# Performance work log

Hardware: AMD Instinct MI355X
Metric: run time of the kernel (lower is better)

## Reference

```python
import jax, jax.numpy as jnp
import numpy as np

SDIM, VDIM, HID, DEPTH = 128, 3, 64, 4
N, E = 50000, 800000
CUTOFF = 5.0


def setup_inputs() -> dict:
    key = jax.random.key(0)
    ks = jax.random.split(key, 16)
    s = jax.random.normal(ks[0], (N, SDIM), jnp.float32)
    v = jax.random.normal(ks[1], (N, 3, VDIM), jnp.float32)
    edge_index = jax.random.randint(ks[2], (2, E), 0, N, dtype=jnp.int32).astype(jnp.int64)
    d = jax.random.uniform(ks[3], (E,), jnp.float32) * CUTOFF
    r = jax.random.normal(ks[4], (E, 3), jnp.float32)
    r = r / jnp.linalg.norm(r, axis=-1, keepdims=True)
    batch = jnp.zeros((N,), jnp.int64)

    def w(k, shape):
        return jax.random.normal(k, shape, jnp.float32) / jnp.sqrt(jnp.float32(shape[-2]))

    return {
        's': s, 'v': v, 'edge_index': edge_index, 'd': d, 'r': r, 'batch': batch,
        'We1': w(ks[5], (DEPTH, 2 * SDIM + 1, HID)), 'be1': jnp.zeros((DEPTH, HID), jnp.float32),
        'We2': w(ks[6], (DEPTH, HID, HID)), 'be2': jnp.zeros((DEPTH, HID), jnp.float32),
        'Wn1': w(ks[7], (DEPTH, SDIM + HID, HID)), 'bn1': jnp.zeros((DEPTH, HID), jnp.float32),
        'Wn2': w(ks[8], (DEPTH, HID, SDIM)), 'bn2': jnp.zeros((DEPTH, SDIM), jnp.float32),
        'Wv': w(ks[9], (DEPTH, HID, 2 * VDIM)), 'bv': jnp.zeros((DEPTH, 2 * VDIM), jnp.float32),
    }


def _egcl(s, v, src, dst, d, r, C, deg, We1, be1, We2, be2, Wn1, bn1, Wn2, bn2, Wv, bv):
    n = s.shape[0]
    # edge message MLP on gathered endpoint features + distance
    x = jnp.concatenate([s[dst], s[src], d[:, None]], axis=-1)   # [E, 2*SDIM+1]
    h = jax.nn.silu(x @ We1 + be1)
    h = jax.nn.silu(h @ We2 + be2)
    h = h * C[:, None]                                            # cutoff envelope
    # scalar update
    agg_s = jax.ops.segment_sum(h, dst, num_segments=n)           # [N, HID]
    u = jax.nn.silu(jnp.concatenate([s, agg_s], axis=-1) @ Wn1 + bn1)
    s = s + (u @ Wn2 + bn2)
    # equivariant vector update: gated neighbor vectors + gated edge directions
    gates = h @ Wv + bv                                           # [E, 2*VDIM]
    g1, g2 = gates[:, :VDIM], gates[:, VDIM:]
    mv = v[src] * g1[:, None, :] + r[:, :, None] * g2[:, None, :] # [E, 3, VDIM]
    agg_v = jax.ops.segment_sum(mv, dst, num_segments=n) / deg[:, None, None]  # mean aggr
    v = v + agg_v
    return s, v


def reference(s, v, edge_index, d, r, batch, We1, be1, We2, be2, Wn1, bn1, Wn2, bn2, Wv, bv):
    src, dst = edge_index[0], edge_index[1]
    C = 0.5 * (jnp.cos(jnp.pi * d / CUTOFF) + 1.0) * (d < CUTOFF).astype(d.dtype)
    deg = jax.ops.segment_sum(jnp.ones_like(d), dst, num_segments=s.shape[0])
    deg = jnp.maximum(deg, 1.0)
    for i in range(DEPTH):
        s, v = _egcl(s, v, src, dst, d, r, C, deg,
                     We1[i], be1[i], We2[i], be2[i],
                     Wn1[i], bn1[i], Wn2[i], bn2[i], Wv[i], bv[i])
    return (s, v)
```

## Files before the change

### kernel.cpp

```cpp
#include <hip/hip_runtime.h>
#include <math.h>

#define SDIM 128
#define HID 64
#define DEPTH 4
#define CUTOFF_F 5.0f
#define CHUNK 4096

typedef __attribute__((ext_vector_type(8))) short bf16x8;
typedef __attribute__((ext_vector_type(4))) float f32x4;
typedef float4 __attribute__((aligned(4))) float4_u;

__device__ __forceinline__ float silu_f(float x) {
    float e = __expf(-x);
    return x * __builtin_amdgcn_rcpf(1.0f + e);
}

__device__ __forceinline__ unsigned short f2bf(float x) {
    __bf16 b = (__bf16)x;
    return __builtin_bit_cast(unsigned short, b);
}
__device__ __forceinline__ unsigned int f2bf2(float a, float b) {
    return (unsigned int)f2bf(a) | ((unsigned int)f2bf(b) << 16);
}
// ... 92 lines not shown
    for (int base = base0; base < base0 + CHUNK; base += 256) {
        int i = base + t;
        int v = (i < N) ? deg_i[i] : 0;
        int incl = v;
#pragma unroll
        for (int off = 1; off < 64; off <<= 1) {
            int x = __shfl_up(incl, off, 64);
            if (lane >= off) incl += x;
        }
        if (lane == 63) wsum[w] = incl;
        __syncthreads();
        int wpre = 0;
#pragma unroll
        for (int k = 0; k < 4; ++k) if (k < w) wpre += wsum[k];
        int total = wsum[0] + wsum[1] + wsum[2] + wsum[3];
        int carry = carry_s;
        if (i < N) row_start[i] = carry + wpre + incl - v;
        __syncthreads();
        if (t == 0) carry_s = carry + total;
        __syncthreads();
    }
}

__global__ void scatter_kernel(const int* __restrict__ srcw, const int* __restrict__ dstw,
                               const float* __restrict__ dvec, const float* __restrict__ rvec,
                               const int* __restrict__ row_start, int* __restrict__ cursor,
                               float* __restrict__ rec, int E) {
    int e = blockIdx.x * blockDim.x + threadIdx.x;
    if (e >= E) return;
    int dd = dstw[e];
    int ofs = atomicAdd(&cursor[dd], 1);
    int pos = row_start[dd] + ofs;
    float dv = dvec[e];
    float c = 0.5f * (cosf(3.14159265358979323846f * dv * (1.0f / CUTOFF_F)) + 1.0f);
    c = (dv < CUTOFF_F) ? c : 0.0f;
    float4 r0 = make_float4(__int_as_float(srcw[e]), __int_as_float(dd), dv, c);
    float4 r1 = make_float4(rvec[(size_t)e * 3 + 0], rvec[(size_t)e * 3 + 1],
                            rvec[(size_t)e * 3 + 2], 0.0f);
    *(float4*)(rec + (size_t)pos * 8)     = r0;
    *(float4*)(rec + (size_t)pos * 8 + 4) = r1;
}

__global__ __launch_bounds__(256) void wprep_kernel(
    const float* __restrict__ We1, const float* __restrict__ We2,
    const float* __restrict__ Wv,  const float* __restrict__ Wn1,
    const float* __restrict__ Wn2,
    unsigned short* __restrict__ We1t, unsigned short* __restrict__ We2t,
    unsigned short* __restrict__ Wvt,  unsigned short* __restrict__ Wn1t,
    unsigned short* __restrict__ Wn2t) {
    int l = blockIdx.x, t = threadIdx.x;
    const float* W2 = We2 + (size_t)l * HID * HID;
    unsigned short* T2 = We2t + (size_t)l * HID * HID;
    for (int idx = t; idx < HID * HID; idx += 256) {
        int n = idx >> 6, k = idx & 63;
        T2[n * 64 + k] = f2bf(W2[k * HID + n]);
    }
    const float* Wvl = Wv + (size_t)l * HID * 6;
    unsigned short* Tv = Wvt + (size_t)l * 16 * 64;
    for (int idx = t; idx < 16 * 64; idx += 256) {
        int n = idx >> 6, k = idx & 63;
        Tv[idx] = (n < 6) ? f2bf(Wvl[k * 6 + n]) : (unsigned short)0;
    }
    const float* W1 = We1 + (size_t)l * 257 * 64;
    unsigned short* T1 = We1t + (size_t)l * 128 * 128;
    for (int idx = t; idx < 128 * 128; idx += 256) {
        int n = idx >> 7, k = idx & 127;
        float w = (n < 64) ? W1[(size_t)k * 64 + n] : W1[(size_t)(k + 128) * 64 + (n - 64)];
        T1[n * 128 + k] = f2bf(w);
    }
    const float* Wn1l = Wn1 + (size_t)l * 192 * 64;
    unsigned short* Tn1 = Wn1t + (size_t)l * 64 * 192;
    for (int idx = t; idx < 64 * 192; idx += 256) {
        int n = idx / 192, k = idx - n * 192;
        Tn1[idx] = f2bf(Wn1l[(size_t)k * 64 + n]);
    }
    const float* Wn2l = Wn2 + (size_t)l * 64 * 128;
    unsigned short* Tn2 = Wn2t + (size_t)l * 128 * 64;
    for (int idx = t; idx < 128 * 64; idx += 256) {
        int n = idx >> 6, k = idx & 63;
        Tn2[idx] = f2bf(Wn2l[(size_t)k * 128 + n]);
    }
}

__global__ __launch_bounds__(256) void node_pre_kernel(
    const float* __restrict__ s, const unsigned short* __restrict__ We1t,
    const float* __restrict__ be1,
    unsigned short* __restrict__ Pa, unsigned short* __restrict__ Pb, int N)
{
    __shared__ unsigned short sa[4][16 * 136];
    int t = threadIdx.x;
    int lane = t & 63, w = t >> 6;
    int n0 = blockIdx.x * 64;
    int m0 = w * 16;
    unsigned short* sw = sa[w];
    for (int idx = lane; idx < 512; idx += 64) {
        int rl = idx >> 5, c4 = (idx & 31) << 2;
        int n = n0 + m0 + rl;
        float4 val = make_float4(0.f, 0.f, 0.f, 0.f);
        if (n < N) val = *(const float4*)(s + (size_t)n * SDIM + c4);
        *(uint2*)(sw + rl * 136 + c4) = make_uint2(f2bf2(val.x, val.y), f2bf2(val.z, val.w));
    }
    __builtin_amdgcn_wave_barrier();
    int lm = lane & 15, lq = lane >> 4;

    bf16x8 af[4];
#pragma unroll
    for (int kc = 0; kc < 4; ++kc)
        af[kc] = *(const bf16x8*)(sw + lm * 136 + kc * 32 + lq * 8);

#pragma unroll
    for (int ct = 0; ct < 8; ++ct) {
        int col = ct * 16 + lm;
        f32x4 acc = {0.f, 0.f, 0.f, 0.f};
#pragma unroll
        for (int kc = 0; kc < 4; ++kc) {
            bf16x8 b = *(const bf16x8*)(We1t + (size_t)col * 128 + kc * 32 + lq * 8);
            acc = __builtin_amdgcn_mfma_f32_16x16x32_bf16(af[kc], b, acc, 0, 0, 0);
        }
        float bias = (ct < 4) ? be1[col] : 0.0f;
#pragma unroll
        for (int g = 0; g < 4; ++g) {
            int n = n0 + m0 + lq * 4 + g;
            if (n < N) {
                if (ct < 4) Pa[(size_t)n * HID + col]        = f2bf(acc[g] + bias);
                else        Pb[(size_t)n * HID + (col - 64)] = f2bf(acc[g]);
            }
        }
    }
}

__global__ __launch_bounds__(256) void edge_kernel(
    const float* __restrict__ rec,
    const unsigned short* __restrict__ Pa, const unsigned short* __restrict__ Pb,
    const float* __restrict__ wd,
    const unsigned short* __restrict__ We2t, const float* __restrict__ be2,
    const unsigned short* __restrict__ Wvt, const float* __restrict__ bv,
    const float* __restrict__ v,
    float* __restrict__ agg_s, float* __restrict__ agg_v, int E)
{
    __shared__ unsigned short hb[64 * 72];
    __shared__ float  gl[64 * 8];
    __shared__ float  vb[64 * 12];
    __shared__ int    m_dst[64];
    __shared__ float  m_C[64];
    __shared__ float4 m_r4[64];
    int t = threadIdx.x;
    int e0 = blockIdx.x * 64;
    int lane = t & 63, w = t >> 6;
    int lm = lane & 15, lq = lane >> 4;
    int m0 = w * 16, rm = m0 + lm;
    int ka = lq * 8, kb = 32 + lq * 8;

    int e  = e0 + rm;
    int ec = min(e, E - 1);
    float4 r0 = *(const float4*)(rec + (size_t)ec * 8);
    int srcr = __float_as_int(r0.x);
    int dstr = __float_as_int(r0.y);
    float dv = r0.z;
    float Cr = (e < E) ? r0.w : 0.0f;

    const unsigned short* pa = Pa + (size_t)dstr * HID;
    const unsigned short* pb = Pb + (size_t)srcr * HID;
    bf16x8 ba0 = *(const bf16x8*)(pa + ka);
    bf16x8 bb0 = *(const bf16x8*)(pb + ka);
    bf16x8 ba1 = *(const bf16x8*)(pa + kb);
    bf16x8 bb1 = *(const bf16x8*)(pb + kb);
    f8 xw = load8(wd + ka), yw = load8(wd + kb);

    if (lq == 0) {
        m_dst[rm] = dstr;
        m_C[rm]   = Cr;
        m_r4[rm]  = *(const float4*)(rec + (size_t)ec * 8 + 4);
    }
    {
        const float* vr = v + (size_t)srcr * 9;
        if (lq < 2) {
            float4_u a = *(const float4_u*)(vr + lq * 4);
            *(float4*)(vb + rm * 12 + lq * 4) = make_float4(a.x, a.y, a.z, a.w);
        } else if (lq == 2) {
            vb[rm * 12 + 8] = vr[8];
        }
    }
    bf16x8 wv0 = *(const bf16x8*)(Wvt + (size_t)lm * 64 + ka);
    bf16x8 wv1 = *(const bf16x8*)(Wvt + (size_t)lm * 64 + kb);

    bf16x8 afr0, afr1;
    {
        float fa[8], fb[8], h1[8];
        unpack8(ba0, fa); unpack8(bb0, fb);
#pragma unroll
        for (int j = 0; j < 8; ++j) h1[j] = silu_f(fa[j] + fb[j] + dv * xw.v[j]);
        afr0 = pack8(h1);
        unpack8(ba1, fa); unpack8(bb1, fb);
#pragma unroll
        for (int j = 0; j < 8; ++j) h1[j] = silu_f(fa[j] + fb[j] + dv * yw.v[j]);
        afr1 = pack8(h1);
    }

    __builtin_amdgcn_wave_barrier();
    float cc[4];
#pragma unroll
    for (int g = 0; g < 4; ++g) cc[g] = m_C[m0 + lq * 4 + g];
#pragma unroll
    for (int t4 = 0; t4 < 4; ++t4) {
        int col = t4 * 16 + lm;
        bf16x8 b0 = *(const bf16x8*)(We2t + (size_t)col * 64 + ka);
        bf16x8 b1 = *(const bf16x8*)(We2t + (size_t)col * 64 + kb);
        f32x4 a = {0.f, 0.f, 0.f, 0.f};
        a = __builtin_amdgcn_mfma_f32_16x16x32_bf16(afr0, b0, a, 0, 0, 0);
        a = __builtin_amdgcn_mfma_f32_16x16x32_bf16(afr1, b1, a, 0, 0, 0);
        float bias = be2[col];
#pragma unroll
        for (int g = 0; g < 4; ++g) {
            int er = m0 + lq * 4 + g;
            hb[er * 72 + col] = f2bf(silu_f(a[g] + bias) * cc[g]);
        }
    }
    __builtin_amdgcn_wave_barrier();

    {
        bf16x8 hb0 = *(const bf16x8*)(hb + rm * 72 + ka);
        bf16x8 hb1 = *(const bf16x8*)(hb + rm * 72 + kb);
        f32x4 ga = {0.f, 0.f, 0.f, 0.f};
        ga = __builtin_amdgcn_mfma_f32_16x16x32_bf16(wv0, hb0, ga, 0, 0, 0);
        ga = __builtin_amdgcn_mfma_f32_16x16x32_bf16(wv1, hb1, ga, 0, 0, 0);
        int er2 = m0 + lm;
        if (lq == 0) {
            float4_u bb = *(const float4_u*)bv;
            *(float4*)(gl + er2 * 8) =
                make_float4(ga[0] + bb.x, ga[1] + bb.y, ga[2] + bb.z, ga[3] + bb.w);
        } else if (lq == 1) {
            gl[er2 * 8 + 4] = ga[0] + bv[4];
            gl[er2 * 8 + 5] = ga[1] + bv[5];
        }
    }

    {
        int c = lane;
        float acc = 0.f;
        int cur = m_dst[m0];
#pragma unroll 4
        for (int r = m0; r < m0 + 16; ++r) {
            int dr = m_dst[r];
            if (dr != cur) {
                atomicAdd(&agg_s[(size_t)cur * HID + c], acc);
                acc = 0.f; cur = dr;
            }
            acc += bf2f(hb[r * 72 + c]);
        }
        atomicAdd(&agg_s[(size_t)cur * HID + c], acc);
    }
    __builtin_amdgcn_wave_barrier();

    if (lane < 36) {
        int seg = lane / 9;
        int c = lane - seg * 9;
        int i = c / 3, j = c - i * 3;
        int r0v = m0 + seg * 4;
        const float* mrf = (const float*)m_r4;
        float acc = 0.f;
        int cur = m_dst[r0v];
#pragma unroll
        for (int r = 0; r < 4; ++r) {
            int rr = r0v + r;
            int dr = m_dst[rr];
            if (dr != cur) {
                atomicAdd(&agg_v[(size_t)cur * 9 + c], acc);
                acc = 0.f; cur = dr;
            }
            if (e0 + rr < E) {
                acc += vb[rr * 12 + c] * gl[rr * 8 + j]
                     + mrf[rr * 4 + i] * gl[rr * 8 + 3 + j];
            }
        }
        atomicAdd(&agg_v[(size_t)cur * 9 + c], acc);
    }
}

__global__ __launch_bounds__(256) void node_fused_kernel(
    float* __restrict__ s, float* __restrict__ vout,
    float* __restrict__ agg_s, float* __restrict__ agg_v,
    const int* __restrict__ row_start,
    const unsigned short* __restrict__ Wn1t, const float* __restrict__ bn1,
    const unsigned short* __restrict__ Wn2t, const float* __restrict__ bn2,
    const unsigned short* __restrict__ We1tn, const float* __restrict__ be1n,
    unsigned short* __restrict__ Pa, unsigned short* __restrict__ Pb,
    int N, int do_pre)
{
    __shared__ unsigned short xa[4][16 * 200];
    __shared__ unsigned short ub[64 * 72];
    int t = threadIdx.x;
    int lane = t & 63, w = t >> 6;
    int n0 = blockIdx.x * 64;
    int m0 = w * 16;
    unsigned short* xw = xa[w];

    for (int idx = lane; idx < 512; idx += 64) {
        int rl = idx >> 5, c4 = (idx & 31) << 2;
        int n = n0 + m0 + rl;
        float4 val = make_float4(0.f, 0.f, 0.f, 0.f);
        if (n < N) val = *(const float4*)(s + (size_t)n * SDIM + c4);
        *(uint2*)(xw + rl * 200 + c4) = make_uint2(f2bf2(val.x, val.y), f2bf2(val.z, val.w));
    }
    for (int idx = lane; idx < 256; idx += 64) {
        int rl = idx >> 4, c4 = (idx & 15) << 2;
        int n = n0 + m0 + rl;
        float4 val = make_float4(0.f, 0.f, 0.f, 0.f);
        if (n < N) {
            float* ap = agg_s + (size_t)n * HID + c4;
            val = *(const float4*)ap;
            *(float4*)ap = make_float4(0.f, 0.f, 0.f, 0.f);
        }
        *(uint2*)(xw + rl * 200 + 128 + c4) = make_uint2(f2bf2(val.x, val.y), f2bf2(val.z, val.w));
    }
    __builtin_amdgcn_wave_barrier();

    int lm = lane & 15, lq = lane >> 4;

    bf16x8 af[6];
#pragma unroll
    for (int kc = 0; kc < 6; ++kc)
        af[kc] = *(const bf16x8*)(xw + lm * 200 + kc * 32 + lq * 8);

#pragma unroll
    for (int ct = 0; ct < 4; ++ct) {
        int col = ct * 16 + lm;
        f32x4 acc = {0.f, 0.f, 0.f, 0.f};
#pragma unroll
        for (int kc = 0; kc < 6; ++kc) {
            bf16x8 b = *(const bf16x8*)(Wn1t + (size_t)col * 192 + kc * 32 + lq * 8);
            acc = __builtin_amdgcn_mfma_f32_16x16x32_bf16(af[kc], b, acc, 0, 0, 0);
        }
        float bias = bn1[col];
#pragma unroll
        for (int g = 0; g < 4; ++g) {
            int er = m0 + lq * 4 + g;
            ub[er * 72 + col] = f2bf(silu_f(acc[g] + bias));
        }
    }
    __builtin_amdgcn_wave_barrier();

    unsigned short* sa = xw;
    bf16x8 uf[2];
#pragma unroll
    for (int kc = 0; kc < 2; ++kc)
        uf[kc] = *(const bf16x8*)(ub + (m0 + lm) * 72 + kc * 32 + lq * 8);

#pragma unroll
    for (int ct = 0; ct < 8; ++ct) {
        int col = ct * 16 + lm;
        f32x4 acc = {0.f, 0.f, 0.f, 0.f};
#pragma unroll
        for (int kc = 0; kc < 2; ++kc) {
            bf16x8 b = *(const bf16x8*)(Wn2t + (size_t)col * 64 + kc * 32 + lq * 8);
            acc = __builtin_amdgcn_mfma_f32_16x16x32_bf16(uf[kc], b, acc, 0, 0, 0);
        }
        float bias = bn2[col];
#pragma unroll
        for (int g = 0; g < 4; ++g) {
            int erl = lq * 4 + g;
            int n = n0 + m0 + erl;
            if (n < N) {
                float* sp = s + (size_t)n * SDIM + col;
                float sv = *sp + acc[g] + bias;
                *sp = sv;
                sa[erl * 136 + col] = f2bf(sv);
            } else {
                sa[erl * 136 + col] = 0;
            }
        }
    }
    __builtin_amdgcn_wave_barrier();

    if (do_pre) {
        bf16x8 pf[4];
#pragma unroll
        for (int kc = 0; kc < 4; ++kc)
            pf[kc] = *(const bf16x8*)(sa + lm * 136 + kc * 32 + lq * 8);

#pragma unroll
        for (int ct = 0; ct < 8; ++ct) {
            int col = ct * 16 + lm;
            f32x4 acc = {0.f, 0.f, 0.f, 0.f};
#pragma unroll
            for (int kc = 0; kc < 4; ++kc) {
                bf16x8 b = *(const bf16x8*)(We1tn + (size_t)col * 128 + kc * 32 + lq * 8);
                acc = __builtin_amdgcn_mfma_f32_16x16x32_bf16(pf[kc], b, acc, 0, 0, 0);
            }
            float bias = (ct < 4) ? be1n[col] : 0.0f;
#pragma unroll
            for (int g = 0; g < 4; ++g) {
                int n = n0 + m0 + lq * 4 + g;
                if (n < N) {
                    if (ct < 4) Pa[(size_t)n * HID + col]        = f2bf(acc[g] + bias);
                    else        Pb[(size_t)n * HID + (col - 64)] = f2bf(acc[g]);
                }
            }
        }
    }

    for (int idx = lane; idx < 144; idx += 64) {
        int rl = idx / 9, c = idx - rl * 9;
        int n2 = n0 + m0 + rl;
        if (n2 < N) {
            float av = agg_v[(size_t)n2 * 9 + c];
            agg_v[(size_t)n2 * 9 + c] = 0.f;
            float dg = fmaxf((float)(row_start[n2 + 1] - row_start[n2]), 1.0f);
            vout[(size_t)n2 * 9 + c] += av / dg;
        }
    }
}

extern "C" void kernel_launch(void* const* d_in, const int* in_sizes, int n_in,
                              void* d_out, int out_size, void* d_ws, size_t ws_size,
                              hipStream_t stream)
{
    const float* s_in  = (const float*)d_in[0];
    const float* v_in  = (const float*)d_in[1];
    const void*  ei    = d_in[2];
    const float* d_vec = (const float*)d_in[3];
    const float* r_vec = (const float*)d_in[4];
    const float* We1 = (const float*)d_in[6];
    const float* be1 = (const float*)d_in[7];
    const float* We2 = (const float*)d_in[8];
    const float* be2 = (const float*)d_in[9];
    const float* Wn1 = (const float*)d_in[10];
    const float* bn1 = (const float*)d_in[11];
    const float* Wn2 = (const float*)d_in[12];
    const float* bn2 = (const float*)d_in[13];
    const float* Wv  = (const float*)d_in[14];
    const float* bv  = (const float*)d_in[15];

    int N = in_sizes[0] / SDIM;
    int E = in_sizes[3];

    float* out_s = (float*)d_out;
    float* out_v = out_s + (size_t)N * SDIM;

    char* wp = (char*)d_ws;
    auto alloc = [&wp](size_t bytes) -> char* {
        char* p = wp;
        wp += (bytes + 31) & ~(size_t)31;
        return p;
    };
    float* rec       = (float*)alloc((size_t)E * 8 * 4);
    unsigned short* Pa = (unsigned short*)alloc((size_t)N * HID * 2);
    unsigned short* Pb = (unsigned short*)alloc((size_t)N * HID * 2);
    float* agg_s     = (float*)alloc((size_t)N * HID * 4);
    float* agg_v     = (float*)alloc((size_t)N * 9 * 4);
    int*   deg_i     = (int*)alloc((size_t)N * 4);
    int*   cursor    = (int*)alloc((size_t)N * 4);
    int*   row_start = (int*)alloc((size_t)(N + 1) * 4);
    int*   part      = (int*)alloc(64 * 4);
    int*   flag      = (int*)alloc(16);
    int*   srcw      = (int*)alloc((size_t)E * 4);
    int*   dstw      = (int*)alloc((size_t)E * 4);
    unsigned short* We2t = (unsigned short*)alloc((size_t)DEPTH * HID * HID * 2);
    unsigned short* Wvt  = (unsigned short*)alloc((size_t)DEPTH * 16 * 64 * 2);
    unsigned short* We1t = (unsigned short*)alloc((size_t)DEPTH * 128 * 128 * 2);
    unsigned short* Wn1t = (unsigned short*)alloc((size_t)DEPTH * 64 * 192 * 2);
    unsigned short* Wn2t = (unsigned short*)alloc((size_t)DEPTH * 128 * 64 * 2);

    hipMemcpyAsync(out_s, s_in, (size_t)N * SDIM * sizeof(float),
                   hipMemcpyDeviceToDevice, stream);
    hipMemcpyAsync(out_v, v_in, (size_t)N * 9 * sizeof(float),
                   hipMemcpyDeviceToDevice, stream);

    detect_idx_kernel<<<1, 64, 0, stream>>>(ei, N, flag);
    hipMemsetAsync(deg_i, 0, (size_t)N * 2 * sizeof(int), stream);
    hipMemsetAsync(agg_s, 0, (size_t)N * (HID + 9) * sizeof(float), stream);
    decode_idx_kernel<<<(2 * E + 255) / 256, 256, 0, stream>>>(ei, E, N, flag,
                                                               srcw, dstw, deg_i);
    int B1 = (N + CHUNK - 1) / CHUNK;
    scan1_kernel<<<B1, 256, 0, stream>>>(deg_i, part, N);
    scan2_kernel<<<1, 64, 0, stream>>>(part, row_start, B1, N);
    scan3_kernel<<<B1, 256, 0, stream>>>(deg_i, part, row_start, N);
    scatter_kernel<<<(E + 255) / 256, 256, 0, stream>>>(srcw, dstw, d_vec, r_vec,
                                                        row_start, cursor, rec, E);
    wprep_kernel<<<DEPTH, 256, 0, stream>>>(We1, We2, Wv, Wn1, Wn2,
                                            We1t, We2t, Wvt, Wn1t, Wn2t);

    int nb_n = (N + 63) / 64;
    int nb_e = (E + 63) / 64;
    node_pre_kernel<<<nb_n, 256, 0, stream>>>(out_s, We1t, be1, Pa, Pb, N);
    for (int l = 0; l < DEPTH; ++l) {
        int ln = (l + 1 < DEPTH) ? (l + 1) : 0;
        const float* We1_l = We1 + (size_t)l * 257 * 64;
        const float* be2_l = be2 + (size_t)l * 64;
        const float* bn1_l = bn1 + (size_t)l * 64;
        const float* bn2_l = bn2 + (size_t)l * 128;
        const float* bv_l  = bv  + (size_t)l * 6;
        const float* be1_n = be1 + (size_t)ln * 64;
        const unsigned short* We2t_l = We2t + (size_t)l * HID * HID;
        const unsigned short* Wvt_l  = Wvt  + (size_t)l * 16 * 64;
        const unsigned short* Wn1t_l = Wn1t + (size_t)l * 64 * 192;
        const unsigned short* Wn2t_l = Wn2t + (size_t)l * 128 * 64;
        const unsigned short* We1t_n = We1t + (size_t)ln * 128 * 128;

        edge_kernel<<<nb_e, 256, 0, stream>>>(rec, Pa, Pb,
                                              We1_l + 256 * 64,
                                              We2t_l, be2_l, Wvt_l, bv_l,
                                              out_v, agg_s, agg_v, E);
        node_fused_kernel<<<nb_n, 256, 0, stream>>>(out_s, out_v, agg_s, agg_v,
                                                    row_start,
                                                    Wn1t_l, bn1_l, Wn2t_l, bn2_l,
                                                    We1t_n, be1_n, Pa, Pb,
                                                    N, (l + 1 < DEPTH) ? 1 : 0);
    }
}
```

Baseline: 815.3 us.

## Make edge kernel persistent with double-buffered gather prefetch; shrink node blocks

```diff
diff --git a/kernel.cpp b/kernel.cpp
--- a/kernel.cpp
+++ b/kernel.cpp
@@ -198,23 +198,20 @@
     }
 }
 
-__global__ __launch_bounds__(256) void node_pre_kernel(
+__global__ __launch_bounds__(64) void node_pre_kernel(
     const float* __restrict__ s, const unsigned short* __restrict__ We1t,
     const float* __restrict__ be1,
     unsigned short* __restrict__ Pa, unsigned short* __restrict__ Pb, int N)
 {
-    __shared__ unsigned short sa[4][16 * 136];
-    int t = threadIdx.x;
-    int lane = t & 63, w = t >> 6;
-    int n0 = blockIdx.x * 64;
-    int m0 = w * 16;
-    unsigned short* sw = sa[w];
+    __shared__ unsigned short sa[16 * 136];
+    int lane = threadIdx.x;
+    int n0 = blockIdx.x * 16;
     for (int idx = lane; idx < 512; idx += 64) {
         int rl = idx >> 5, c4 = (idx & 31) << 2;
-        int n = n0 + m0 + rl;
+        int n = n0 + rl;
         float4 val = make_float4(0.f, 0.f, 0.f, 0.f);
         if (n < N) val = *(const float4*)(s + (size_t)n * SDIM + c4);
-        *(uint2*)(sw + rl * 136 + c4) = make_uint2(f2bf2(val.x, val.y), f2bf2(val.z, val.w));
+        *(uint2*)(sa + rl * 136 + c4) = make_uint2(f2bf2(val.x, val.y), f2bf2(val.z, val.w));
     }
     __builtin_amdgcn_wave_barrier();
     int lm = lane & 15, lq = lane >> 4;
@@ -222,7 +219,7 @@
     bf16x8 af[4];
 #pragma unroll
     for (int kc = 0; kc < 4; ++kc)
-        af[kc] = *(const bf16x8*)(sw + lm * 136 + kc * 32 + lq * 8);
+        af[kc] = *(const bf16x8*)(sa + lm * 136 + kc * 32 + lq * 8);
 
 #pragma unroll
     for (int ct = 0; ct < 8; ++ct) {
@@ -236,12 +233,44 @@
         float bias = (ct < 4) ? be1[col] : 0.0f;
 #pragma unroll
         for (int g = 0; g < 4; ++g) {
-            int n = n0 + m0 + lq * 4 + g;
+            int n = n0 + lq * 4 + g;
             if (n < N) {
                 if (ct < 4) Pa[(size_t)n * HID + col]        = f2bf(acc[g] + bias);
                 else        Pb[(size_t)n * HID + (col - 64)] = f2bf(acc[g]);
             }
         }
+    }
+}
+
+__device__ __forceinline__ void issue_tile(
+    float4 r0v, bool e_ok, const float* r4p,
+    int rm, int lq, int ka, int kb,
+    const unsigned short* __restrict__ Pa, const unsigned short* __restrict__ Pb,
+    const float* __restrict__ v,
+    bf16x8& ba0, bf16x8& bb0, bf16x8& ba1, bf16x8& bb1, float& dv_out,
+    int* m_dst, float* m_C, float4* m_r4, float* vb)
+{
+    int srcr = __float_as_int(r0v.x);
+    int dstr = __float_as_int(r0v.y);
+    dv_out = r0v.z;
+    float Cr = e_ok ? r0v.w : 0.0f;
+    const unsigned short* pa = Pa + (size_t)dstr * HID;
+    const unsigned short* pb = Pb + (size_t)srcr * HID;
+    ba0 = *(const bf16x8*)(pa + ka);
+    bb0 = *(const bf16x8*)(pb + ka);
+    ba1 = *(const bf16x8*)(pa + kb);
+    bb1 = *(const bf16x8*)(pb + kb);
+    if (lq == 0) {
+        m_dst[rm] = dstr;
+        m_C[rm]   = Cr;
+        m_r4[rm]  = *(const float4*)r4p;
+    }
+    const float* vr = v + (size_t)srcr * 9;
+    if (lq < 2) {
+        float4_u a = *(const float4_u*)(vr + lq * 4);
+        *(float4*)(vb + rm * 12 + lq * 4) = make_float4(a.x, a.y, a.z, a.w);
+    } else if (lq == 2) {
+        vb[rm * 12 + 8] = vr[8];
     }
 }
 
@@ -252,148 +281,155 @@
     const unsigned short* __restrict__ We2t, const float* __restrict__ be2,
     const unsigned short* __restrict__ Wvt, const float* __restrict__ bv,
     const float* __restrict__ v,
-    float* __restrict__ agg_s, float* __restrict__ agg_v, int E)
+    float* __restrict__ agg_s, float* __restrict__ agg_v,
+    int E, int ntiles, int tpb)
 {
     __shared__ unsigned short hb[64 * 72];
     __shared__ float  gl[64 * 8];
-    __shared__ float  vb[64 * 12];
-    __shared__ int    m_dst[64];
-    __shared__ float  m_C[64];
-    __shared__ float4 m_r4[64];
+    __shared__ float  vb2[2][64 * 12];
+    __shared__ int    m_dst2[2][64];
+    __shared__ float  m_C2[2][64];
+    __shared__ float4 m_r42[2][64];
+
     int t = threadIdx.x;
-    int e0 = blockIdx.x * 64;
     int lane = t & 63, w = t >> 6;
     int lm = lane & 15, lq = lane >> 4;
     int m0 = w * 16, rm = m0 + lm;
     int ka = lq * 8, kb = 32 + lq * 8;
 
-    int e  = e0 + rm;
-    int ec = min(e, E - 1);
-    float4 r0 = *(const float4*)(rec + (size_t)ec * 8);
-    int srcr = __float_as_int(r0.x);
-    int dstr = __float_as_int(r0.y);
-    float dv = r0.z;
-    float Cr = (e < E) ? r0.w : 0.0f;
-
-    const unsigned short* pa = Pa + (size_t)dstr * HID;
-    const unsigned short* pb = Pb + (size_t)srcr * HID;
-    bf16x8 ba0 = *(const bf16x8*)(pa + ka);
-    bf16x8 bb0 = *(const bf16x8*)(pb + ka);
-    bf16x8 ba1 = *(const bf16x8*)(pa + kb);
-    bf16x8 bb1 = *(const bf16x8*)(pb + kb);
+    int t0 = blockIdx.x * tpb;
+    int t1 = min(t0 + tpb, ntiles);
+    if (t0 >= t1) return;
+
     f8 xw = load8(wd + ka), yw = load8(wd + kb);
-
-    if (lq == 0) {
-        m_dst[rm] = dstr;
-        m_C[rm]   = Cr;
-        m_r4[rm]  = *(const float4*)(rec + (size_t)ec * 8 + 4);
-    }
-    {
-        const float* vr = v + (size_t)srcr * 9;
-        if (lq < 2) {
-            float4_u a = *(const float4_u*)(vr + lq * 4);
-            *(float4*)(vb + rm * 12 + lq * 4) = make_float4(a.x, a.y, a.z, a.w);
-        } else if (lq == 2) {
-            vb[rm * 12 + 8] = vr[8];
-        }
-    }
     bf16x8 wv0 = *(const bf16x8*)(Wvt + (size_t)lm * 64 + ka);
     bf16x8 wv1 = *(const bf16x8*)(Wvt + (size_t)lm * 64 + kb);
-
-    bf16x8 afr0, afr1;
+    float4_u bvv = *(const float4_u*)bv;
+    float bv4 = bv[4], bv5 = bv[5];
+
+    bf16x8 ba0, bb0, ba1, bb1;
+    float dv;
     {
-        float fa[8], fb[8], h1[8];
-        unpack8(ba0, fa); unpack8(bb0, fb);
-#pragma unroll
-        for (int j = 0; j < 8; ++j) h1[j] = silu_f(fa[j] + fb[j] + dv * xw.v[j]);
-        afr0 = pack8(h1);
-        unpack8(ba1, fa); unpack8(bb1, fb);
-#pragma unroll
-        for (int j = 0; j < 8; ++j) h1[j] = silu_f(fa[j] + fb[j] + dv * yw.v[j]);
-        afr1 = pack8(h1);
-    }
-
-    __builtin_amdgcn_wave_barrier();
-    float cc[4];
-#pragma unroll
-    for (int g = 0; g < 4; ++g) cc[g] = m_C[m0 + lq * 4 + g];
-#pragma unroll
-    for (int t4 = 0; t4 < 4; ++t4) {
-        int col = t4 * 16 + lm;
-        bf16x8 b0 = *(const bf16x8*)(We2t + (size_t)col * 64 + ka);
-        bf16x8 b1 = *(const bf16x8*)(We2t + (size_t)col * 64 + kb);
-        f32x4 a = {0.f, 0.f, 0.f, 0.f};
-        a = __builtin_amdgcn_mfma_f32_16x16x32_bf16(afr0, b0, a, 0, 0, 0);
-        a = __builtin_amdgcn_mfma_f32_16x16x32_bf16(afr1, b1, a, 0, 0, 0);
-        float bias = be2[col];
-#pragma unroll
-        for (int g = 0; g < 4; ++g) {
-            int er = m0 + lq * 4 + g;
-            hb[er * 72 + col] = f2bf(silu_f(a[g] + bias) * cc[g]);
-        }
-    }
-    __builtin_amdgcn_wave_barrier();
-
-    {
-        bf16x8 hb0 = *(const bf16x8*)(hb + rm * 72 + ka);
-        bf16x8 hb1 = *(const bf16x8*)(hb + rm * 72 + kb);
-        f32x4 ga = {0.f, 0.f, 0.f, 0.f};
-        ga = __builtin_amdgcn_mfma_f32_16x16x32_bf16(wv0, hb0, ga, 0, 0, 0);
-        ga = __builtin_amdgcn_mfma_f32_16x16x32_bf16(wv1, hb1, ga, 0, 0, 0);
-        int er2 = m0 + lm;
-        if (lq == 0) {
-            float4_u bb = *(const float4_u*)bv;
-            *(float4*)(gl + er2 * 8) =
-                make_float4(ga[0] + bb.x, ga[1] + bb.y, ga[2] + bb.z, ga[3] + bb.w);
-        } else if (lq == 1) {
-            gl[er2 * 8 + 4] = ga[0] + bv[4];
-            gl[er2 * 8 + 5] = ga[1] + bv[5];
-        }
-    }
-
-    {
-        int c = lane;
-        float acc = 0.f;
-        int cur = m_dst[m0];
+        int e  = t0 * 64 + rm;
+        int ec = min(e, E - 1);
+        float4 r0 = *(const float4*)(rec + (size_t)ec * 8);
+        int par0 = t0 & 1;
+        issue_tile(r0, e < E, rec + (size_t)ec * 8 + 4, rm, lq, ka, kb, Pa, Pb, v,
+                   ba0, bb0, ba1, bb1, dv,
+                   m_dst2[par0], m_C2[par0], m_r42[par0], vb2[par0]);
+    }
+
+    for (int itl = t0; itl < t1; ++itl) {
+        int par = itl & 1, npar = par ^ 1;
+        bool hasnext = (itl + 1 < t1);
+        int en  = (itl + 1) * 64 + rm;
+        int ecn = min(en, E - 1);
+        float4 r0n;
+        if (hasnext) r0n = *(const float4*)(rec + (size_t)ecn * 8);
+
+        bf16x8 afr0, afr1;
+        {
+            float fa[8], fb[8], h1[8];
+            unpack8(ba0, fa); unpack8(bb0, fb);
+#pragma unroll
+            for (int j = 0; j < 8; ++j) h1[j] = silu_f(fa[j] + fb[j] + dv * xw.v[j]);
+            afr0 = pack8(h1);
+            unpack8(ba1, fa); unpack8(bb1, fb);
+#pragma unroll
+            for (int j = 0; j < 8; ++j) h1[j] = silu_f(fa[j] + fb[j] + dv * yw.v[j]);
+            afr1 = pack8(h1);
+        }
+
+        float cc[4];
+#pragma unroll
+        for (int g = 0; g < 4; ++g) cc[g] = m_C2[par][m0 + lq * 4 + g];
+#pragma unroll
+        for (int t4 = 0; t4 < 4; ++t4) {
+            int col = t4 * 16 + lm;
+            bf16x8 b0 = *(const bf16x8*)(We2t + (size_t)col * 64 + ka);
+            bf16x8 b1 = *(const bf16x8*)(We2t + (size_t)col * 64 + kb);
+            f32x4 a = {0.f, 0.f, 0.f, 0.f};
+            a = __builtin_amdgcn_mfma_f32_16x16x32_bf16(afr0, b0, a, 0, 0, 0);
+            a = __builtin_amdgcn_mfma_f32_16x16x32_bf16(afr1, b1, a, 0, 0, 0);
+            float bias = be2[col];
+#pragma unroll
+            for (int g = 0; g < 4; ++g) {
+                int er = m0 + lq * 4 + g;
+                hb[er * 72 + col] = f2bf(silu_f(a[g] + bias) * cc[g]);
+            }
+        }
+        __builtin_amdgcn_wave_barrier();
+
+        {
+            bf16x8 hb0 = *(const bf16x8*)(hb + rm * 72 + ka);
+            bf16x8 hb1 = *(const bf16x8*)(hb + rm * 72 + kb);
+            f32x4 ga = {0.f, 0.f, 0.f, 0.f};
+            ga = __builtin_amdgcn_mfma_f32_16x16x32_bf16(wv0, hb0, ga, 0, 0, 0);
+            ga = __builtin_amdgcn_mfma_f32_16x16x32_bf16(wv1, hb1, ga, 0, 0, 0);
+            int er2 = m0 + lm;
+            if (lq == 0) {
+                *(float4*)(gl + er2 * 8) =
+                    make_float4(ga[0] + bvv.x, ga[1] + bvv.y, ga[2] + bvv.z, ga[3] + bvv.w);
+            } else if (lq == 1) {
+                gl[er2 * 8 + 4] = ga[0] + bv4;
+                gl[er2 * 8 + 5] = ga[1] + bv5;
+            }
+        }
+
+        if (hasnext) {
+            issue_tile(r0n, en < E, rec + (size_t)ecn * 8 + 4, rm, lq, ka, kb, Pa, Pb, v,
+                       ba0, bb0, ba1, bb1, dv,
+                       m_dst2[npar], m_C2[npar], m_r42[npar], vb2[npar]);
+        }
+
+        {
+            int c = lane;
+            const int* md = m_dst2[par];
+            float acc = 0.f;
+            int cur = md[m0];
 #pragma unroll 4
-        for (int r = m0; r < m0 + 16; ++r) {
-            int dr = m_dst[r];
-            if (dr != cur) {
-                atomicAdd(&agg_s[(size_t)cur * HID + c], acc);
-                acc = 0.f; cur = dr;
-            }
-            acc += bf2f(hb[r * 72 + c]);
-        }
-        atomicAdd(&agg_s[(size_t)cur * HID + c], acc);
-    }
-    __builtin_amdgcn_wave_barrier();
-
-    if (lane < 36) {
-        int seg = lane / 9;
-        int c = lane - seg * 9;
-        int i = c / 3, j = c - i * 3;
-        int r0v = m0 + seg * 4;
-        const float* mrf = (const float*)m_r4;
-        float acc = 0.f;
-        int cur = m_dst[r0v];
-#pragma unroll
-        for (int r = 0; r < 4; ++r) {
-            int rr = r0v + r;
-            int dr = m_dst[rr];
-            if (dr != cur) {
-                atomicAdd(&agg_v[(size_t)cur * 9 + c], acc);
-                acc = 0.f; cur = dr;
-            }
-            if (e0 + rr < E) {
-                acc += vb[rr * 12 + c] * gl[rr * 8 + j]
-                     + mrf[rr * 4 + i] * gl[rr * 8 + 3 + j];
-            }
-        }
-        atomicAdd(&agg_v[(size_t)cur * 9 + c], acc);
-    }
-}
-
-__global__ __launch_bounds__(256) void node_fused_kernel(
+            for (int r = m0; r < m0 + 16; ++r) {
+                int dr = md[r];
+                if (dr != cur) {
+                    atomicAdd(&agg_s[(size_t)cur * HID + c], acc);
+                    acc = 0.f; cur = dr;
+                }
+                acc += bf2f(hb[r * 72 + c]);
+            }
+            atomicAdd(&agg_s[(size_t)cur * HID + c], acc);
+        }
+        __builtin_amdgcn_wave_barrier();
+
+        if (lane < 36) {
+            int seg = lane / 9;
+            int c = lane - seg * 9;
+            int i = c / 3, j = c - i * 3;
+            int r0v = m0 + seg * 4;
+            const float* mrf = (const float*)m_r42[par];
+            const float* vbp = vb2[par];
+            const int* md = m_dst2[par];
+            float acc = 0.f;
+            int cur = md[r0v];
+#pragma unroll
+            for (int r = 0; r < 4; ++r) {
+                int rr = r0v + r;
+                int dr = md[rr];
+                if (dr != cur) {
+                    atomicAdd(&agg_v[(size_t)cur * 9 + c], acc);
+                    acc = 0.f; cur = dr;
+                }
+                if (itl * 64 + rr < E) {
+                    acc += vbp[rr * 12 + c] * gl[rr * 8 + j]
+                         + mrf[rr * 4 + i] * gl[rr * 8 + 3 + j];
+                }
+            }
+            atomicAdd(&agg_v[(size_t)cur * 9 + c], acc);
+        }
+        __builtin_amdgcn_wave_barrier();
+    }
+}
+
+__global__ __launch_bounds__(64) void node_fused_kernel(
     float* __restrict__ s, float* __restrict__ vout,
     float* __restrict__ agg_s, float* __restrict__ agg_v,
     const int* __restrict__ row_start,
@@ -403,31 +439,39 @@
     unsigned short* __restrict__ Pa, unsigned short* __restrict__ Pb,
     int N, int do_pre)
 {
-    __shared__ unsigned short xa[4][16 * 200];
-    __shared__ unsigned short ub[64 * 72];
-    int t = threadIdx.x;
-    int lane = t & 63, w = t >> 6;
-    int n0 = blockIdx.x * 64;
-    int m0 = w * 16;
-    unsigned short* xw = xa[w];
+    __shared__ unsigned short xa[16 * 200];
+    __shared__ unsigned short ub[16 * 72];
+    int lane = threadIdx.x;
+    int n0 = blockIdx.x * 16;
+
+    for (int idx = lane; idx < 144; idx += 64) {
+        int rl = idx / 9, c = idx - rl * 9;
+        int n2 = n0 + rl;
+        if (n2 < N) {
+            float av = agg_v[(size_t)n2 * 9 + c];
+            agg_v[(size_t)n2 * 9 + c] = 0.f;
+            float dg = fmaxf((float)(row_start[n2 + 1] - row_start[n2]), 1.0f);
+            vout[(size_t)n2 * 9 + c] += av / dg;
+        }
+    }
 
     for (int idx = lane; idx < 512; idx += 64) {
         int rl = idx >> 5, c4 = (idx & 31) << 2;
-        int n = n0 + m0 + rl;
+        int n = n0 + rl;
         float4 val = make_float4(0.f, 0.f, 0.f, 0.f);
         if (n < N) val = *(const float4*)(s + (size_t)n * SDIM + c4);
-        *(uint2*)(xw + rl * 200 + c4) = make_uint2(f2bf2(val.x, val.y), f2bf2(val.z, val.w));
+        *(uint2*)(xa + rl * 200 + c4) = make_uint2(f2bf2(val.x, val.y), f2bf2(val.z, val.w));
     }
     for (int idx = lane; idx < 256; idx += 64) {
         int rl = idx >> 4, c4 = (idx & 15) << 2;
-        int n = n0 + m0 + rl;
+        int n = n0 + rl;
         float4 val = make_float4(0.f, 0.f, 0.f, 0.f);
         if (n < N) {
             float* ap = agg_s + (size_t)n * HID + c4;
             val = *(const float4*)ap;
             *(float4*)ap = make_float4(0.f, 0.f, 0.f, 0.f);
         }
-        *(uint2*)(xw + rl * 200 + 128 + c4) = make_uint2(f2bf2(val.x, val.y), f2bf2(val.z, val.w));
+        *(uint2*)(xa + rl * 200 + 128 + c4) = make_uint2(f2bf2(val.x, val.y), f2bf2(val.z, val.w));
     }
     __builtin_amdgcn_wave_barrier();
 
@@ -436,7 +480,7 @@
     bf16x8 af[6];
 #pragma unroll
     for (int kc = 0; kc < 6; ++kc)
-        af[kc] = *(const bf16x8*)(xw + lm * 200 + kc * 32 + lq * 8);
+        af[kc] = *(const bf16x8*)(xa + lm * 200 + kc * 32 + lq * 8);
 
 #pragma unroll
     for (int ct = 0; ct < 4; ++ct) {
@@ -450,17 +494,27 @@
         float bias = bn1[col];
 #pragma unroll
         for (int g = 0; g < 4; ++g) {
-            int er = m0 + lq * 4 + g;
+            int er = lq * 4 + g;
             ub[er * 72 + col] = f2bf(silu_f(acc[g] + bias));
         }
     }
     __builtin_amdgcn_wave_barrier();
 
-    unsigned short* sa = xw;
+    unsigned short* sa = xa;
     bf16x8 uf[2];
 #pragma unroll
     for (int kc = 0; kc < 2; ++kc)
-        uf[kc] = *(const bf16x8*)(ub + (m0 + lm) * 72 + kc * 32 + lq * 8);
+        uf[kc] = *(const bf16x8*)(ub + lm * 72 + kc * 32 + lq * 8);
+
+    float sld[32];
+#pragma unroll
+    for (int ct = 0; ct < 8; ++ct) {
+#pragma unroll
+        for (int g = 0; g < 4; ++g) {
+            int n = n0 + lq * 4 + g;
+            sld[ct * 4 + g] = (n < N) ? s[(size_t)n * SDIM + ct * 16 + lm] : 0.0f;
+        }
+    }
 
 #pragma unroll
     for (int ct = 0; ct < 8; ++ct) {
@@ -475,11 +529,10 @@
 #pragma unroll
         for (int g = 0; g < 4; ++g) {
             int erl = lq * 4 + g;
-            int n = n0 + m0 + erl;
+            int n = n0 + erl;
             if (n < N) {
-                float* sp = s + (size_t)n * SDIM + col;
-                float sv = *sp + acc[g] + bias;
-                *sp = sv;
+                float sv = sld[ct * 4 + g] + acc[g] + bias;
+                s[(size_t)n * SDIM + col] = sv;
                 sa[erl * 136 + col] = f2bf(sv);
             } else {
                 sa[erl * 136 + col] = 0;
@@ -506,23 +559,12 @@
             float bias = (ct < 4) ? be1n[col] : 0.0f;
 #pragma unroll
             for (int g = 0; g < 4; ++g) {
-                int n = n0 + m0 + lq * 4 + g;
+                int n = n0 + lq * 4 + g;
                 if (n < N) {
                     if (ct < 4) Pa[(size_t)n * HID + col]        = f2bf(acc[g] + bias);
                     else        Pb[(size_t)n * HID + (col - 64)] = f2bf(acc[g]);
                 }
             }
-        }
-    }
-
-    for (int idx = lane; idx < 144; idx += 64) {
-        int rl = idx / 9, c = idx - rl * 9;
-        int n2 = n0 + m0 + rl;
-        if (n2 < N) {
-            float av = agg_v[(size_t)n2 * 9 + c];
-            agg_v[(size_t)n2 * 9 + c] = 0.f;
-            float dg = fmaxf((float)(row_start[n2 + 1] - row_start[n2]), 1.0f);
-            vout[(size_t)n2 * 9 + c] += av / dg;
         }
     }
 }
@@ -596,9 +638,12 @@
     wprep_kernel<<<DEPTH, 256, 0, stream>>>(We1, We2, Wv, Wn1, Wn2,
                                             We1t, We2t, Wvt, Wn1t, Wn2t);
 
-    int nb_n = (N + 63) / 64;
-    int nb_e = (E + 63) / 64;
-    node_pre_kernel<<<nb_n, 256, 0, stream>>>(out_s, We1t, be1, Pa, Pb, N);
+    int nb_n = (N + 15) / 16;
+    int ntiles = (E + 63) / 64;
+    int tpb = (ntiles + 2047) / 2048;
+    int nb_e = (ntiles + tpb - 1) / tpb;
+
+    node_pre_kernel<<<nb_n, 64, 0, stream>>>(out_s, We1t, be1, Pa, Pb, N);
     for (int l = 0; l < DEPTH; ++l) {
         int ln = (l + 1 < DEPTH) ? (l + 1) : 0;
         const float* We1_l = We1 + (size_t)l * 257 * 64;
@@ -616,11 +661,12 @@
         edge_kernel<<<nb_e, 256, 0, stream>>>(rec, Pa, Pb,
                                               We1_l + 256 * 64,
                                               We2t_l, be2_l, Wvt_l, bv_l,
-                                              out_v, agg_s, agg_v, E);
-        node_fused_kernel<<<nb_n, 256, 0, stream>>>(out_s, out_v, agg_s, agg_v,
-                                                    row_start,
-                                                    Wn1t_l, bn1_l, Wn2t_l, bn2_l,
-                                                    We1t_n, be1_n, Pa, Pb,
-                                                    N, (l + 1 < DEPTH) ? 1 : 0);
-    }
-}
+                                              out_v, agg_s, agg_v,
+                                              E, ntiles, tpb);
+        node_fused_kernel<<<nb_n, 64, 0, stream>>>(out_s, out_v, agg_s, agg_v,
+                                                   row_start,
+                                                   Wn1t_l, bn1_l, Wn2t_l, bn2_l,
+                                                   We1t_n, be1_n, Pa, Pb,
+                                                   N, (l + 1 < DEPTH) ? 1 : 0);
+    }
+}
```

Result: no change. 809.6 us (-0.7%).

## Transpose MFMA operands for row-contiguous stores and shrink node blocks to one wave

Applied to the files above, without the earlier changes.

```diff
diff --git a/kernel.cpp b/kernel.cpp
--- a/kernel.cpp
+++ b/kernel.cpp
@@ -198,48 +198,48 @@
     }
 }
 
-__global__ __launch_bounds__(256) void node_pre_kernel(
+__global__ __launch_bounds__(64) void node_pre_kernel(
     const float* __restrict__ s, const unsigned short* __restrict__ We1t,
     const float* __restrict__ be1,
     unsigned short* __restrict__ Pa, unsigned short* __restrict__ Pb, int N)
 {
-    __shared__ unsigned short sa[4][16 * 136];
-    int t = threadIdx.x;
-    int lane = t & 63, w = t >> 6;
-    int n0 = blockIdx.x * 64;
-    int m0 = w * 16;
-    unsigned short* sw = sa[w];
+    __shared__ unsigned short sa[16 * 136];
+    int lane = threadIdx.x;
+    int n0 = blockIdx.x * 16;
     for (int idx = lane; idx < 512; idx += 64) {
         int rl = idx >> 5, c4 = (idx & 31) << 2;
-        int n = n0 + m0 + rl;
+        int n = n0 + rl;
         float4 val = make_float4(0.f, 0.f, 0.f, 0.f);
         if (n < N) val = *(const float4*)(s + (size_t)n * SDIM + c4);
-        *(uint2*)(sw + rl * 136 + c4) = make_uint2(f2bf2(val.x, val.y), f2bf2(val.z, val.w));
+        *(uint2*)(sa + rl * 136 + c4) = make_uint2(f2bf2(val.x, val.y), f2bf2(val.z, val.w));
     }
     __builtin_amdgcn_wave_barrier();
     int lm = lane & 15, lq = lane >> 4;
+    int nr = n0 + lm;
+    bool rowok = (nr < N);
 
     bf16x8 af[4];
 #pragma unroll
     for (int kc = 0; kc < 4; ++kc)
-        af[kc] = *(const bf16x8*)(sw + lm * 136 + kc * 32 + lq * 8);
+        af[kc] = *(const bf16x8*)(sa + lm * 136 + kc * 32 + lq * 8);
 
 #pragma unroll
     for (int ct = 0; ct < 8; ++ct) {
-        int col = ct * 16 + lm;
         f32x4 acc = {0.f, 0.f, 0.f, 0.f};
 #pragma unroll
         for (int kc = 0; kc < 4; ++kc) {
-            bf16x8 b = *(const bf16x8*)(We1t + (size_t)col * 128 + kc * 32 + lq * 8);
-            acc = __builtin_amdgcn_mfma_f32_16x16x32_bf16(af[kc], b, acc, 0, 0, 0);
-        }
-        float bias = (ct < 4) ? be1[col] : 0.0f;
-#pragma unroll
-        for (int g = 0; g < 4; ++g) {
-            int n = n0 + m0 + lq * 4 + g;
-            if (n < N) {
-                if (ct < 4) Pa[(size_t)n * HID + col]        = f2bf(acc[g] + bias);
-                else        Pb[(size_t)n * HID + (col - 64)] = f2bf(acc[g]);
+            bf16x8 b = *(const bf16x8*)(We1t + (size_t)(ct * 16 + lm) * 128 + kc * 32 + lq * 8);
+            acc = __builtin_amdgcn_mfma_f32_16x16x32_bf16(b, af[kc], acc, 0, 0, 0);
+        }
+        if (rowok) {
+            if (ct < 4) {
+                float4 b4 = *(const float4*)(be1 + ct * 16 + lq * 4);
+                *(uint2*)(Pa + (size_t)nr * HID + ct * 16 + lq * 4) =
+                    make_uint2(f2bf2(acc[0] + b4.x, acc[1] + b4.y),
+                               f2bf2(acc[2] + b4.z, acc[3] + b4.w));
+            } else {
+                *(uint2*)(Pb + (size_t)nr * HID + (ct - 4) * 16 + lq * 4) =
+                    make_uint2(f2bf2(acc[0], acc[1]), f2bf2(acc[2], acc[3]));
             }
         }
     }
@@ -258,7 +258,6 @@
     __shared__ float  gl[64 * 8];
     __shared__ float  vb[64 * 12];
     __shared__ int    m_dst[64];
-    __shared__ float  m_C[64];
     __shared__ float4 m_r4[64];
     int t = threadIdx.x;
     int e0 = blockIdx.x * 64;
@@ -285,7 +284,6 @@
 
     if (lq == 0) {
         m_dst[rm] = dstr;
-        m_C[rm]   = Cr;
         m_r4[rm]  = *(const float4*)(rec + (size_t)ec * 8 + 4);
     }
     {
@@ -313,24 +311,17 @@
         afr1 = pack8(h1);
     }
 
-    __builtin_amdgcn_wave_barrier();
-    float cc[4];
-#pragma unroll
-    for (int g = 0; g < 4; ++g) cc[g] = m_C[m0 + lq * 4 + g];
 #pragma unroll
     for (int t4 = 0; t4 < 4; ++t4) {
-        int col = t4 * 16 + lm;
-        bf16x8 b0 = *(const bf16x8*)(We2t + (size_t)col * 64 + ka);
-        bf16x8 b1 = *(const bf16x8*)(We2t + (size_t)col * 64 + kb);
+        bf16x8 a0 = *(const bf16x8*)(We2t + (size_t)(t4 * 16 + lm) * 64 + ka);
+        bf16x8 a1 = *(const bf16x8*)(We2t + (size_t)(t4 * 16 + lm) * 64 + kb);
         f32x4 a = {0.f, 0.f, 0.f, 0.f};
-        a = __builtin_amdgcn_mfma_f32_16x16x32_bf16(afr0, b0, a, 0, 0, 0);
-        a = __builtin_amdgcn_mfma_f32_16x16x32_bf16(afr1, b1, a, 0, 0, 0);
-        float bias = be2[col];
-#pragma unroll
-        for (int g = 0; g < 4; ++g) {
-            int er = m0 + lq * 4 + g;
-            hb[er * 72 + col] = f2bf(silu_f(a[g] + bias) * cc[g]);
-        }
+        a = __builtin_amdgcn_mfma_f32_16x16x32_bf16(a0, afr0, a, 0, 0, 0);
+        a = __builtin_amdgcn_mfma_f32_16x16x32_bf16(a1, afr1, a, 0, 0, 0);
+        float4 b4 = *(const float4*)(be2 + t4 * 16 + lq * 4);
+        unsigned int p0 = f2bf2(silu_f(a[0] + b4.x) * Cr, silu_f(a[1] + b4.y) * Cr);
+        unsigned int p1 = f2bf2(silu_f(a[2] + b4.z) * Cr, silu_f(a[3] + b4.w) * Cr);
+        *(uint2*)(hb + rm * 72 + t4 * 16 + lq * 4) = make_uint2(p0, p1);
     }
     __builtin_amdgcn_wave_barrier();
 
@@ -393,7 +384,7 @@
     }
 }
 
-__global__ __launch_bounds__(256) void node_fused_kernel(
+__global__ __launch_bounds__(64) void node_fused_kernel(
     float* __restrict__ s, float* __restrict__ vout,
     float* __restrict__ agg_s, float* __restrict__ agg_v,
     const int* __restrict__ row_start,
@@ -403,87 +394,97 @@
     unsigned short* __restrict__ Pa, unsigned short* __restrict__ Pb,
     int N, int do_pre)
 {
-    __shared__ unsigned short xa[4][16 * 200];
-    __shared__ unsigned short ub[64 * 72];
-    int t = threadIdx.x;
-    int lane = t & 63, w = t >> 6;
-    int n0 = blockIdx.x * 64;
-    int m0 = w * 16;
-    unsigned short* xw = xa[w];
+    __shared__ unsigned short xa[16 * 200];
+    __shared__ unsigned short ub[16 * 72];
+    int lane = threadIdx.x;
+    int n0 = blockIdx.x * 16;
+
+    for (int idx = lane; idx < 144; idx += 64) {
+        int rl = idx / 9, c = idx - rl * 9;
+        int n2 = n0 + rl;
+        if (n2 < N) {
+            float av = agg_v[(size_t)n2 * 9 + c];
+            agg_v[(size_t)n2 * 9 + c] = 0.f;
+            float dg = fmaxf((float)(row_start[n2 + 1] - row_start[n2]), 1.0f);
+            vout[(size_t)n2 * 9 + c] += av / dg;
+        }
+    }
 
     for (int idx = lane; idx < 512; idx += 64) {
         int rl = idx >> 5, c4 = (idx & 31) << 2;
-        int n = n0 + m0 + rl;
+        int n = n0 + rl;
         float4 val = make_float4(0.f, 0.f, 0.f, 0.f);
         if (n < N) val = *(const float4*)(s + (size_t)n * SDIM + c4);
-        *(uint2*)(xw + rl * 200 + c4) = make_uint2(f2bf2(val.x, val.y), f2bf2(val.z, val.w));
+        *(uint2*)(xa + rl * 200 + c4) = make_uint2(f2bf2(val.x, val.y), f2bf2(val.z, val.w));
     }
     for (int idx = lane; idx < 256; idx += 64) {
         int rl = idx >> 4, c4 = (idx & 15) << 2;
-        int n = n0 + m0 + rl;
+        int n = n0 + rl;
         float4 val = make_float4(0.f, 0.f, 0.f, 0.f);
         if (n < N) {
             float* ap = agg_s + (size_t)n * HID + c4;
             val = *(const float4*)ap;
             *(float4*)ap = make_float4(0.f, 0.f, 0.f, 0.f);
         }
-        *(uint2*)(xw + rl * 200 + 128 + c4) = make_uint2(f2bf2(val.x, val.y), f2bf2(val.z, val.w));
+        *(uint2*)(xa + rl * 200 + 128 + c4) = make_uint2(f2bf2(val.x, val.y), f2bf2(val.z, val.w));
     }
     __builtin_amdgcn_wave_barrier();
 
     int lm = lane & 15, lq = lane >> 4;
+    int nr = n0 + lm;
+    bool rowok = (nr < N);
 
     bf16x8 af[6];
 #pragma unroll
     for (int kc = 0; kc < 6; ++kc)
-        af[kc] = *(const bf16x8*)(xw + lm * 200 + kc * 32 + lq * 8);
+        af[kc] = *(const bf16x8*)(xa + lm * 200 + kc * 32 + lq * 8);
 
 #pragma unroll
     for (int ct = 0; ct < 4; ++ct) {
-        int col = ct * 16 + lm;
         f32x4 acc = {0.f, 0.f, 0.f, 0.f};
 #pragma unroll
         for (int kc = 0; kc < 6; ++kc) {
-            bf16x8 b = *(const bf16x8*)(Wn1t + (size_t)col * 192 + kc * 32 + lq * 8);
-            acc = __builtin_amdgcn_mfma_f32_16x16x32_bf16(af[kc], b, acc, 0, 0, 0);
-        }
-        float bias = bn1[col];
-#pragma unroll
-        for (int g = 0; g < 4; ++g) {
-            int er = m0 + lq * 4 + g;
-            ub[er * 72 + col] = f2bf(silu_f(acc[g] + bias));
-        }
+            bf16x8 b = *(const bf16x8*)(Wn1t + (size_t)(ct * 16 + lm) * 192 + kc * 32 + lq * 8);
+            acc = __builtin_amdgcn_mfma_f32_16x16x32_bf16(b, af[kc], acc, 0, 0, 0);
+        }
+        float4 b4 = *(const float4*)(bn1 + ct * 16 + lq * 4);
+        unsigned int p0 = f2bf2(silu_f(acc[0] + b4.x), silu_f(acc[1] + b4.y));
+        unsigned int p1 = f2bf2(silu_f(acc[2] + b4.z), silu_f(acc[3] + b4.w));
+        *(uint2*)(ub + lm * 72 + ct * 16 + lq * 4) = make_uint2(p0, p1);
     }
     __builtin_amdgcn_wave_barrier();
 
-    unsigned short* sa = xw;
+    unsigned short* sa = xa;
     bf16x8 uf[2];
 #pragma unroll
     for (int kc = 0; kc < 2; ++kc)
-        uf[kc] = *(const bf16x8*)(ub + (m0 + lm) * 72 + kc * 32 + lq * 8);
+        uf[kc] = *(const bf16x8*)(ub + lm * 72 + kc * 32 + lq * 8);
+
+    float4 sld[8];
+#pragma unroll
+    for (int ct = 0; ct < 8; ++ct)
+        sld[ct] = rowok ? *(const float4*)(s + (size_t)nr * SDIM + ct * 16 + lq * 4)
+                        : make_float4(0.f, 0.f, 0.f, 0.f);
 
 #pragma unroll
     for (int ct = 0; ct < 8; ++ct) {
-        int col = ct * 16 + lm;
         f32x4 acc = {0.f, 0.f, 0.f, 0.f};
 #pragma unroll
         for (int kc = 0; kc < 2; ++kc) {
-            bf16x8 b = *(const bf16x8*)(Wn2t + (size_t)col * 64 + kc * 32 + lq * 8);
-            acc = __builtin_amdgcn_mfma_f32_16x16x32_bf16(uf[kc], b, acc, 0, 0, 0);
-        }
-        float bias = bn2[col];
-#pragma unroll
-        for (int g = 0; g < 4; ++g) {
-            int erl = lq * 4 + g;
-            int n = n0 + m0 + erl;
-            if (n < N) {
-                float* sp = s + (size_t)n * SDIM + col;
-                float sv = *sp + acc[g] + bias;
-                *sp = sv;
-                sa[erl * 136 + col] = f2bf(sv);
-            } else {
-                sa[erl * 136 + col] = 0;
-            }
+            bf16x8 b = *(const bf16x8*)(Wn2t + (size_t)(ct * 16 + lm) * 64 + kc * 32 + lq * 8);
+            acc = __builtin_amdgcn_mfma_f32_16x16x32_bf16(b, uf[kc], acc, 0, 0, 0);
+        }
+        float4 b4 = *(const float4*)(bn2 + ct * 16 + lq * 4);
+        if (rowok) {
+            float4 sv = make_float4(sld[ct].x + acc[0] + b4.x,
+                                    sld[ct].y + acc[1] + b4.y,
+                                    sld[ct].z + acc[2] + b4.z,
+                                    sld[ct].w + acc[3] + b4.w);
+            *(float4*)(s + (size_t)nr * SDIM + ct * 16 + lq * 4) = sv;
+            *(uint2*)(sa + lm * 136 + ct * 16 + lq * 4) =
+                make_uint2(f2bf2(sv.x, sv.y), f2bf2(sv.z, sv.w));
+        } else {
+            *(uint2*)(sa + lm * 136 + ct * 16 + lq * 4) = make_uint2(0u, 0u);
         }
     }
     __builtin_amdgcn_wave_barrier();
@@ -496,33 +497,23 @@
 
 #pragma unroll
         for (int ct = 0; ct < 8; ++ct) {
-            int col = ct * 16 + lm;
             f32x4 acc = {0.f, 0.f, 0.f, 0.f};
 #pragma unroll
             for (int kc = 0; kc < 4; ++kc) {
-                bf16x8 b = *(const bf16x8*)(We1tn + (size_t)col * 128 + kc * 32 + lq * 8);
-                acc = __builtin_amdgcn_mfma_f32_16x16x32_bf16(pf[kc], b, acc, 0, 0, 0);
+                bf16x8 b = *(const bf16x8*)(We1tn + (size_t)(ct * 16 + lm) * 128 + kc * 32 + lq * 8);
+                acc = __builtin_amdgcn_mfma_f32_16x16x32_bf16(b, pf[kc], acc, 0, 0, 0);
             }
-            float bias = (ct < 4) ? be1n[col] : 0.0f;
-#pragma unroll
-            for (int g = 0; g < 4; ++g) {
-                int n = n0 + m0 + lq * 4 + g;
-                if (n < N) {
-                    if (ct < 4) Pa[(size_t)n * HID + col]        = f2bf(acc[g] + bias);
-                    else        Pb[(size_t)n * HID + (col - 64)] = f2bf(acc[g]);
+            if (rowok) {
+                if (ct < 4) {
+                    float4 b4 = *(const float4*)(be1n + ct * 16 + lq * 4);
+                    *(uint2*)(Pa + (size_t)nr * HID + ct * 16 + lq * 4) =
+                        make_uint2(f2bf2(acc[0] + b4.x, acc[1] + b4.y),
+                                   f2bf2(acc[2] + b4.z, acc[3] + b4.w));
+                } else {
+                    *(uint2*)(Pb + (size_t)nr * HID + (ct - 4) * 16 + lq * 4) =
+                        make_uint2(f2bf2(acc[0], acc[1]), f2bf2(acc[2], acc[3]));
                 }
             }
-        }
-    }
-
-    for (int idx = lane; idx < 144; idx += 64) {
-        int rl = idx / 9, c = idx - rl * 9;
-        int n2 = n0 + m0 + rl;
-        if (n2 < N) {
-            float av = agg_v[(size_t)n2 * 9 + c];
-            agg_v[(size_t)n2 * 9 + c] = 0.f;
-            float dg = fmaxf((float)(row_start[n2 + 1] - row_start[n2]), 1.0f);
-            vout[(size_t)n2 * 9 + c] += av / dg;
         }
     }
 }
@@ -596,9 +587,9 @@
     wprep_kernel<<<DEPTH, 256, 0, stream>>>(We1, We2, Wv, Wn1, Wn2,
                                             We1t, We2t, Wvt, Wn1t, Wn2t);
 
-    int nb_n = (N + 63) / 64;
+    int nb_n = (N + 15) / 16;
     int nb_e = (E + 63) / 64;
-    node_pre_kernel<<<nb_n, 256, 0, stream>>>(out_s, We1t, be1, Pa, Pb, N);
+    node_pre_kernel<<<nb_n, 64, 0, stream>>>(out_s, We1t, be1, Pa, Pb, N);
     for (int l = 0; l < DEPTH; ++l) {
         int ln = (l + 1 < DEPTH) ? (l + 1) : 0;
         const float* We1_l = We1 + (size_t)l * 257 * 64;
@@ -617,10 +608,10 @@
                                               We1_l + 256 * 64,
                                               We2t_l, be2_l, Wvt_l, bv_l,
                                               out_v, agg_s, agg_v, E);
-        node_fused_kernel<<<nb_n, 256, 0, stream>>>(out_s, out_v, agg_s, agg_v,
-                                                    row_start,
-                                                    Wn1t_l, bn1_l, Wn2t_l, bn2_l,
-                                                    We1t_n, be1_n, Pa, Pb,
-                                                    N, (l + 1 < DEPTH) ? 1 : 0);
-    }
-}
+        node_fused_kernel<<<nb_n, 64, 0, stream>>>(out_s, out_v, agg_s, agg_v,
+                                                   row_start,
+                                                   Wn1t_l, bn1_l, Wn2t_l, bn2_l,
+                                                   We1t_n, be1_n, Pa, Pb,
+                                                   N, (l + 1 < DEPTH) ? 1 : 0);
+    }
+}
```

New measurement: 789.7 us. 1.03x faster.
